# Kernel tuning notes

Measured on AMD Instinct MI355X. Metric: run time of the kernel, lower is better.

The kernel has to match this reference:

```python
import jax, jax.numpy as jnp
import numpy as np
from jax import lax

HEIGHT, WIDTH = 13, 10
HIDDEN = 256
CONV_OUT = 32 * 3 * 2  # 192, matches torch _get_conv_output_size


def setup_inputs() -> dict:
    key = jax.random.key(0)
    ks = jax.random.split(key, 12)
    B, T = 128, 512
    s = 0.05
    return {
        "x": jax.random.normal(ks[0], (B, T, HEIGHT, WIDTH), jnp.float32),
        "conv1_w": jax.random.normal(ks[1], (16, 1, 3, 3), jnp.float32) * s,
        "conv1_b": jax.random.normal(ks[2], (16,), jnp.float32) * s,
        "conv2_w": jax.random.normal(ks[3], (32, 16, 3, 3), jnp.float32) * s,
        "conv2_b": jax.random.normal(ks[4], (32,), jnp.float32) * s,
        "W_ih": jax.random.normal(ks[5], (4 * HIDDEN, CONV_OUT), jnp.float32) * s,
        "b_ih": jax.random.normal(ks[6], (4 * HIDDEN,), jnp.float32) * s,
        "W_hh": jax.random.normal(ks[7], (4 * HIDDEN, HIDDEN), jnp.float32) * s,
        "b_hh": jax.random.normal(ks[8], (4 * HIDDEN,), jnp.float32) * s,
        "cls_w": jax.random.normal(ks[9], (64, HIDDEN), jnp.float32) * s,
        "cls_b": jax.random.normal(ks[10], (64,), jnp.float32) * s,
    }


def _conv2d(x, w, b):
    # NCHW, OIHW, padding=1 (SAME for 3x3)
    y = lax.conv_general_dilated(x, w, window_strides=(1, 1),
                                 padding=((1, 1), (1, 1)),
                                 dimension_numbers=("NCHW", "OIHW", "NCHW"))
    return y + b[None, :, None, None]


def _maxpool2(x):
    # kernel 2, stride 2, VALID (floor) like nn.MaxPool2d(2)
    return lax.reduce_window(x, -jnp.inf, lax.max,
                             (1, 1, 2, 2), (1, 1, 2, 2), "VALID")


def reference(x, conv1_w, conv1_b, conv2_w, conv2_b, W_ih, b_ih, W_hh, b_hh, cls_w, cls_b):
    B, T, Hd, Wd = x.shape
    xi = x.reshape(B * T, 1, Hd, Wd)
    y = _maxpool2(jax.nn.relu(_conv2d(xi, conv1_w, conv1_b)))
    y = _maxpool2(jax.nn.relu(_conv2d(y, conv2_w, conv2_b)))
    feat = y.reshape(B, T, -1)  # [B, T, 192], channel-major flatten matches torch view

    # Precompute input contribution to gates for all steps (same math, batched)
    gx_all = jnp.einsum("btf,gf->btg", feat, W_ih) + b_ih + b_hh  # [B, T, 4H]
    H = W_hh.shape[1]

    def step(carry, gx):
        h, c = carry
        gates = gx + h @ W_hh.T  # [B, 4H]
        i, f, g, o = jnp.split(gates, 4, axis=1)
        i = jax.nn.sigmoid(i)
        f = jax.nn.sigmoid(f)
        g = jnp.tanh(g)
        o = jax.nn.sigmoid(o)
        c = f * c + i * g
        h = o * jnp.tanh(c)
        return (h, c), None

    h0 = jnp.zeros((B, H), x.dtype)
    c0 = jnp.zeros((B, H), x.dtype)
    (hT, _), _ = lax.scan(step, (h0, c0), jnp.swapaxes(gx_all, 0, 1))
    logits = hT @ cls_w.T + cls_b
    return logits
```

## Files before the change

kernel.cpp:

```cpp
#include <hip/hip_runtime.h>
#include <hip/hip_bf16.h>


typedef _Float16 half2v __attribute__((ext_vector_type(2)));
typedef _Float16 f16x8 __attribute__((ext_vector_type(8)));
typedef float f32x4 __attribute__((ext_vector_type(4)));

__device__ __forceinline__ float dot2f16(half2v a, half2v b, float c) {
#if defined(__has_builtin)
#if __has_builtin(__builtin_amdgcn_fdot2)
    return __builtin_amdgcn_fdot2(a, b, c, false);
#else
    return c + (float)a.x * (float)b.x + (float)a.y * (float)b.y;
#endif
#else
    return c + (float)a.x * (float)b.x + (float)a.y * (float)b.y;
#endif
}

__device__ __forceinline__ unsigned int packf2(const float* p) {
    half2v hv;
    hv.x = (_Float16)p[0];
    hv.y = (_Float16)p[1];
    return __builtin_bit_cast(unsigned int, hv);
}

__device__ __forceinline__ half2v bch2(unsigned int u) {
    return __builtin_bit_cast(half2v, u);
}

__global__ __launch_bounds__(256) void conv_kernel(
    const float* __restrict__ x,
    const float* __restrict__ c1w,
    const float* __restrict__ c1b,
    const float* __restrict__ c2w,
    const float* __restrict__ c2b,
    _Float16* __restrict__ feat)
{
    __shared__ float w1t[9 * 16];
    __shared__ float b1s[16];
    __shared__ float w2t[16 * 9 * 32];
    __shared__ float b2s[32];
    __shared__ float xp[4][14 * 12];
    __shared__ float p1p[4][16 * 8 * 7];

    const int tid = threadIdx.x;

    for (int idx = tid; idx < 144; idx += 256) {
        int oc = idx / 9, k = idx % 9;
        w1t[k * 16 + oc] = c1w[idx];
    }
    if (tid < 16) b1s[tid] = c1b[tid];
    for (int idx = tid; idx < 4608; idx += 256) {
        int oc = idx / 144, ic = (idx / 9) % 16, k = idx % 9;
        w2t[(ic * 9 + k) * 32 + oc] = c2w[idx];
    }
    if (tid < 32) b2s[tid] = c2b[tid];

    const int w = tid >> 6;
    const int lane = tid & 63;
    const int img = blockIdx.x * 4 + w;

    for (int i = lane; i < 14 * 12; i += 64) xp[w][i] = 0.f;
    for (int i = lane; i < 16 * 8 * 7; i += 64) p1p[w][i] = 0.f;
    __syncthreads();

    const float* xin = x + (size_t)img * 130;
    for (int i = lane; i < 130; i += 64) {
        int r = i / 10, c = i % 10;
        xp[w][(r + 1) * 12 + (c + 1)] = xin[i];
    }
    __syncthreads();

    {
        const int oc = lane & 15, q = lane >> 4;
        #pragma unroll
        for (int i = 0; i < 8; i++) {
            int pos = i * 4 + q;
            if (pos < 30) {
                int ph = pos / 5, pw = pos % 5;
                float cmax = -1e30f;
                #pragma unroll
                for (int pt = 0; pt < 4; pt++) {
                    int Y = 2 * ph + (pt >> 1), X = 2 * pw + (pt & 1);
                    float s = 0.f;
                    #pragma unroll
                    for (int k = 0; k < 9; k++) {
                        int dy = k / 3, dx = k % 3;
                        s += w1t[k * 16 + oc] * xp[w][(Y + dy) * 12 + X + dx];
                    }
                    cmax = fmaxf(cmax, s);
                }
                p1p[w][(oc * 8 + ph + 1) * 7 + (pw + 1)] = fmaxf(0.f, cmax + b1s[oc]);
            }
        }
    }
    __syncthreads();

    {
        const int oc = lane & 31, pw2 = lane >> 5;
        float acc[3][4];
        #pragma unroll
        for (int a = 0; a < 3; a++)
            #pragma unroll
            for (int b = 0; b < 4; b++) acc[a][b] = 0.f;

        for (int ic = 0; ic < 16; ic++) {
            #pragma unroll
            for (int k = 0; k < 9; k++) {
                int dy = k / 3, dx = k % 3;
                float wv = w2t[(ic * 9 + k) * 32 + oc];
                #pragma unroll
                for (int ph2 = 0; ph2 < 3; ph2++) {
                    #pragma unroll
                    for (int pt = 0; pt < 4; pt++) {
                        int y = 2 * ph2 + (pt >> 1) + dy;
                        int xx = 2 * pw2 + (pt & 1) + dx;
                        acc[ph2][pt] += wv * p1p[w][(ic * 8 + y) * 7 + xx];
                    }
                }
            }
        }
        float bias = b2s[oc];
        _Float16* fo = feat + (size_t)img * 192;
        #pragma unroll
        for (int ph2 = 0; ph2 < 3; ph2++) {
            float m = fmaxf(fmaxf(acc[ph2][0], acc[ph2][1]),
                            fmaxf(acc[ph2][2], acc[ph2][3]));
            fo[oc * 6 + ph2 * 2 + pw2] = (_Float16)fmaxf(0.f, m + bias);
        }
    }
}

__global__ __launch_bounds__(256) void gemm_gx_kernel(
    const _Float16* __restrict__ feat,
    const float* __restrict__ Wih,
    const float* __restrict__ bih,
    const float* __restrict__ bhh,
    _Float16* __restrict__ gx)
{
    __shared__ uint4 As4[64][25];
    __shared__ uint4 Bs4[64][25];

    const int tid = threadIdx.x;
    const int n0 = blockIdx.x * 64;
    const int m0 = blockIdx.y * 64;

    #pragma unroll
    for (int it = 0; it < 6; it++) {
        int q = tid + it * 256;
        int m = q / 24, c = q % 24;
        As4[m][c] = *(const uint4*)(feat + (size_t)(m0 + m) * 192 + c * 8);
    }
    unsigned int* Bu = (unsigned int*)Bs4;
    #pragma unroll
    for (int it = 0; it < 24; it++) {
        int q = tid + it * 256;
        int n = q / 96, p = q % 96;
        Bu[n * 100 + p] = packf2(Wih + (size_t)(n0 + n) * 192 + 2 * p);
    }
    __syncthreads();

    const int wv = tid >> 6;
    const int lane = tid & 63;
    const int lm = lane & 15;
    const int lk = lane >> 4;

    f32x4 acc[4] = {{0.f, 0.f, 0.f, 0.f}, {0.f, 0.f, 0.f, 0.f},
                    {0.f, 0.f, 0.f, 0.f}, {0.f, 0.f, 0.f, 0.f}};

    #pragma unroll
    for (int ks = 0; ks < 6; ks++) {
        f16x8 a = __builtin_bit_cast(f16x8, As4[wv * 16 + lm][ks * 4 + lk]);
        #pragma unroll
        for (int j = 0; j < 4; j++) {
            f16x8 b = __builtin_bit_cast(f16x8, Bs4[j * 16 + lm][ks * 4 + lk]);
            acc[j] = __builtin_amdgcn_mfma_f32_16x16x32_f16(a, b, acc[j], 0, 0, 0);
        }
    }

    #pragma unroll
    for (int j = 0; j < 4; j++) {
        int n = n0 + j * 16 + lm;
        float bias = bih[n] + bhh[n];
        #pragma unroll
        for (int i = 0; i < 4; i++) {
            int m = m0 + wv * 16 + lk * 4 + i;
            gx[(size_t)m * 1024 + n] = (_Float16)(acc[j][i] + bias);
        }
    }
}

__global__ __attribute__((amdgpu_flat_work_group_size(512, 512), amdgpu_waves_per_eu(2, 2)))
void lstm_kernel(
    const _Float16* __restrict__ gx,
    const float* __restrict__ Whh,
    const float* __restrict__ clsw,
    const float* __restrict__ clsb,
    float* __restrict__ out)
{
    __shared__ uint4 wl4[9][1024];
    __shared__ __align__(16) _Float16 hbuf[2][256];
    __shared__ float hfin[256];
    __shared__ float xg[512];

    const int t = threadIdx.x;
    const int b = blockIdx.x;
    const int r0 = t, r1 = t + 512;

    const float* w0 = Whh + (size_t)r0 * 256;
    const float* w1 = Whh + (size_t)r1 * 256;

    half2v wr0[92], wr1[92];
    #pragma unroll
    for (int p = 0; p < 92; p++) {
        wr0[p] = bch2(packf2(&w0[2 * p]));
        wr1[p] = bch2(packf2(&w1[2 * p]));
    }
    #pragma unroll
    for (int ch = 0; ch < 9; ch++) {
        uint4 v0, v1;
        v0.x = packf2(&w0[184 + 8 * ch + 0]);
        v0.y = packf2(&w0[184 + 8 * ch + 2]);
        v0.z = packf2(&w0[184 + 8 * ch + 4]);
        v0.w = packf2(&w0[184 + 8 * ch + 6]);
        v1.x = packf2(&w1[184 + 8 * ch + 0]);
        v1.y = packf2(&w1[184 + 8 * ch + 2]);
        v1.z = packf2(&w1[184 + 8 * ch + 4]);
        v1.w = packf2(&w1[184 + 8 * ch + 6]);
        wl4[ch][r0] = v0;
        wl4[ch][r1] = v1;
    }
    if (t < 256) hbuf[0][t] = (_Float16)0.f;
    __syncthreads();

    float c = 0.f;
    int cur = 0;
    const _Float16* gxb = gx + (size_t)b * 512 * 1024;
    float ga = (float)gxb[r0];
    float gb = (float)gxb[r1];

    for (int step = 0; step < 512; step++) {
        const _Float16* gxn = gxb + (size_t)((step + 1) & 511) * 1024;
        _Float16 na = gxn[r0];
        _Float16 nb = gxn[r1];

        float acc0 = ga, acc1 = gb;
        const unsigned int* hp = (const unsigned int*)&hbuf[cur][0];

        #pragma unroll
        for (int ch = 0; ch < 23; ch++) {
            uint4 hv = *(const uint4*)(hp + ch * 4);
            unsigned int hw[4] = {hv.x, hv.y, hv.z, hv.w};
            #pragma unroll
            for (int j = 0; j < 4; j++) {
                half2v h2 = bch2(hw[j]);
                acc0 = dot2f16(wr0[ch * 4 + j], h2, acc0);
                acc1 = dot2f16(wr1[ch * 4 + j], h2, acc1);
            }
        }
        #pragma unroll
        for (int ch = 0; ch < 9; ch++) {
            uint4 hv = *(const uint4*)(hp + 92 + 4 * ch);
            uint4 u0 = wl4[ch][r0];
            uint4 u1 = wl4[ch][r1];
            acc0 = dot2f16(bch2(u0.x), bch2(hv.x), acc0);
            acc0 = dot2f16(bch2(u0.y), bch2(hv.y), acc0);
            acc0 = dot2f16(bch2(u0.z), bch2(hv.z), acc0);
            acc0 = dot2f16(bch2(u0.w), bch2(hv.w), acc0);
            acc1 = dot2f16(bch2(u1.x), bch2(hv.x), acc1);
            acc1 = dot2f16(bch2(u1.y), bch2(hv.y), acc1);
            acc1 = dot2f16(bch2(u1.z), bch2(hv.z), acc1);
            acc1 = dot2f16(bch2(u1.w), bch2(hv.w), acc1);
        }

        if (t >= 256) {
            xg[t - 256] = acc0;
            xg[t] = acc1;
        }
        __syncthreads();
        if (t < 256) {
            float i_ = 1.f / (1.f + __expf(-acc0));
            float g_ = 1.f - 2.f / (__expf(2.f * acc1) + 1.f);
            float f_ = 1.f / (1.f + __expf(-xg[t]));
            float o_ = 1.f / (1.f + __expf(-xg[t + 256]));
            c = f_ * c + i_ * g_;
            float th = 1.f - 2.f / (__expf(2.f * c) + 1.f);
            float h = o_ * th;
            hbuf[cur ^ 1][t] = (_Float16)h;
            if (step == 511) hfin[t] = h;
        }
        __syncthreads();
        cur ^= 1;
        ga = (float)na;
        gb = (float)nb;
    }

    if (t < 64) {
        const float* wrow = clsw + t * 256;
        float s = clsb[t];
        for (int k = 0; k < 256; k++) s += wrow[k] * hfin[k];
        out[b * 64 + t] = s;
    }
}

extern "C" void kernel_launch(void* const* d_in, const int* in_sizes, int n_in,
                              void* d_out, int out_size, void* d_ws, size_t ws_size,
                              hipStream_t stream) {
    const float* x    = (const float*)d_in[0];
    const float* c1w  = (const float*)d_in[1];
    const float* c1b  = (const float*)d_in[2];
    const float* c2w  = (const float*)d_in[3];
    const float* c2b  = (const float*)d_in[4];
    const float* Wih  = (const float*)d_in[5];
    const float* bih  = (const float*)d_in[6];
    const float* Whh  = (const float*)d_in[7];
    const float* bhh  = (const float*)d_in[8];
    const float* clsw = (const float*)d_in[9];
    const float* clsb = (const float*)d_in[10];

    _Float16* feat = (_Float16*)d_ws;
    _Float16* gx   = feat + (size_t)65536 * 192;
    float* outp = (float*)d_out;

    hipLaunchKernelGGL(conv_kernel, dim3(16384), dim3(256), 0, stream,
                       x, c1w, c1b, c2w, c2b, feat);
    hipLaunchKernelGGL(gemm_gx_kernel, dim3(16, 1024), dim3(256), 0, stream,
                       feat, Wih, bih, bhh, gx);
    hipLaunchKernelGGL(lstm_kernel, dim3(128), dim3(512), 0, stream,
                       gx, Whh, clsw, clsb, outp);
}
```

Before: 1.329 ms.

## Use one thread per gate row and broadcast hidden state via readlane

The LSTM recurrence kernel now launches 1024 threads per block, one per W_hh row, instead of 512 threads each handling two rows. Every wave loads the hidden state once as a uint2 per lane and broadcasts it with readlane, replacing repeated LDS vector reads of h. Each thread keeps two accumulators that are summed into shared memory. The final h is read from the fp16 buffer instead of a separate fp32 copy, which slightly lowers classifier precision. Register pressure per thread is lower, but more waves contend for the per-step barriers, and readlane produces scalar values that can serialize issue.

```diff
diff --git a/kernel.cpp b/kernel.cpp
--- a/kernel.cpp
+++ b/kernel.cpp
@@ -191,8 +191,7 @@
     }
 }
 
-__global__ __attribute__((amdgpu_flat_work_group_size(512, 512), amdgpu_waves_per_eu(2, 2)))
-void lstm_kernel(
+__global__ __launch_bounds__(1024, 4) void lstm_kernel(
     const _Float16* __restrict__ gx,
     const float* __restrict__ Whh,
     const float* __restrict__ clsw,
@@ -201,35 +200,25 @@
 {
     __shared__ uint4 wl4[9][1024];
     __shared__ __align__(16) _Float16 hbuf[2][256];
-    __shared__ float hfin[256];
-    __shared__ float xg[512];
+    __shared__ float xg[1024];
 
     const int t = threadIdx.x;
     const int b = blockIdx.x;
-    const int r0 = t, r1 = t + 512;
-
-    const float* w0 = Whh + (size_t)r0 * 256;
-    const float* w1 = Whh + (size_t)r1 * 256;
-
-    half2v wr0[92], wr1[92];
-    #pragma unroll
-    for (int p = 0; p < 92; p++) {
-        wr0[p] = bch2(packf2(&w0[2 * p]));
-        wr1[p] = bch2(packf2(&w1[2 * p]));
-    }
+    const int lane = t & 63;
+
+    const float* wrow = Whh + (size_t)t * 256;
+
+    half2v wr[92];
+    #pragma unroll
+    for (int p = 0; p < 92; p++) wr[p] = bch2(packf2(&wrow[2 * p]));
     #pragma unroll
     for (int ch = 0; ch < 9; ch++) {
-        uint4 v0, v1;
-        v0.x = packf2(&w0[184 + 8 * ch + 0]);
-        v0.y = packf2(&w0[184 + 8 * ch + 2]);
-        v0.z = packf2(&w0[184 + 8 * ch + 4]);
-        v0.w = packf2(&w0[184 + 8 * ch + 6]);
-        v1.x = packf2(&w1[184 + 8 * ch + 0]);
-        v1.y = packf2(&w1[184 + 8 * ch + 2]);
-        v1.z = packf2(&w1[184 + 8 * ch + 4]);
-        v1.w = packf2(&w1[184 + 8 * ch + 6]);
-        wl4[ch][r0] = v0;
-        wl4[ch][r1] = v1;
+        uint4 v;
+        v.x = packf2(&wrow[184 + 8 * ch + 0]);
+        v.y = packf2(&wrow[184 + 8 * ch + 2]);
+        v.z = packf2(&wrow[184 + 8 * ch + 4]);
+        v.w = packf2(&wrow[184 + 8 * ch + 6]);
+        wl4[ch][t] = v;
     }
     if (t < 256) hbuf[0][t] = (_Float16)0.f;
     __syncthreads();
@@ -237,69 +226,57 @@
     float c = 0.f;
     int cur = 0;
     const _Float16* gxb = gx + (size_t)b * 512 * 1024;
-    float ga = (float)gxb[r0];
-    float gb = (float)gxb[r1];
+    float ga = (float)gxb[t];
 
     for (int step = 0; step < 512; step++) {
         const _Float16* gxn = gxb + (size_t)((step + 1) & 511) * 1024;
-        _Float16 na = gxn[r0];
-        _Float16 nb = gxn[r1];
-
-        float acc0 = ga, acc1 = gb;
-        const unsigned int* hp = (const unsigned int*)&hbuf[cur][0];
-
-        #pragma unroll
-        for (int ch = 0; ch < 23; ch++) {
-            uint4 hv = *(const uint4*)(hp + ch * 4);
-            unsigned int hw[4] = {hv.x, hv.y, hv.z, hv.w};
-            #pragma unroll
-            for (int j = 0; j < 4; j++) {
-                half2v h2 = bch2(hw[j]);
-                acc0 = dot2f16(wr0[ch * 4 + j], h2, acc0);
-                acc1 = dot2f16(wr1[ch * 4 + j], h2, acc1);
-            }
+        _Float16 na = gxn[t];
+
+        uint2 vh = *(const uint2*)&hbuf[cur][lane * 4];
+
+        float acc0 = ga, acc1 = 0.f;
+        #pragma unroll
+        for (int p = 0; p < 92; p += 2) {
+            unsigned int h0 = __builtin_amdgcn_readlane(vh.x, p >> 1);
+            unsigned int h1 = __builtin_amdgcn_readlane(vh.y, p >> 1);
+            acc0 = dot2f16(wr[p], bch2(h0), acc0);
+            acc1 = dot2f16(wr[p + 1], bch2(h1), acc1);
         }
         #pragma unroll
         for (int ch = 0; ch < 9; ch++) {
-            uint4 hv = *(const uint4*)(hp + 92 + 4 * ch);
-            uint4 u0 = wl4[ch][r0];
-            uint4 u1 = wl4[ch][r1];
-            acc0 = dot2f16(bch2(u0.x), bch2(hv.x), acc0);
-            acc0 = dot2f16(bch2(u0.y), bch2(hv.y), acc0);
-            acc0 = dot2f16(bch2(u0.z), bch2(hv.z), acc0);
-            acc0 = dot2f16(bch2(u0.w), bch2(hv.w), acc0);
-            acc1 = dot2f16(bch2(u1.x), bch2(hv.x), acc1);
-            acc1 = dot2f16(bch2(u1.y), bch2(hv.y), acc1);
-            acc1 = dot2f16(bch2(u1.z), bch2(hv.z), acc1);
-            acc1 = dot2f16(bch2(u1.w), bch2(hv.w), acc1);
-        }
-
-        if (t >= 256) {
-            xg[t - 256] = acc0;
-            xg[t] = acc1;
-        }
+            uint4 u = wl4[ch][t];
+            int p = 92 + 4 * ch;
+            unsigned int h0 = __builtin_amdgcn_readlane(vh.x, (p >> 1) + 0);
+            unsigned int h1 = __builtin_amdgcn_readlane(vh.y, (p >> 1) + 0);
+            unsigned int h2 = __builtin_amdgcn_readlane(vh.x, (p >> 1) + 1);
+            unsigned int h3 = __builtin_amdgcn_readlane(vh.y, (p >> 1) + 1);
+            acc0 = dot2f16(bch2(u.x), bch2(h0), acc0);
+            acc1 = dot2f16(bch2(u.y), bch2(h1), acc1);
+            acc0 = dot2f16(bch2(u.z), bch2(h2), acc0);
+            acc1 = dot2f16(bch2(u.w), bch2(h3), acc1);
+        }
+        xg[t] = acc0 + acc1;
         __syncthreads();
+
         if (t < 256) {
-            float i_ = 1.f / (1.f + __expf(-acc0));
-            float g_ = 1.f - 2.f / (__expf(2.f * acc1) + 1.f);
-            float f_ = 1.f / (1.f + __expf(-xg[t]));
-            float o_ = 1.f / (1.f + __expf(-xg[t + 256]));
+            float i_ = 1.f / (1.f + __expf(-xg[t]));
+            float f_ = 1.f / (1.f + __expf(-xg[t + 256]));
+            float g_ = 1.f - 2.f / (__expf(2.f * xg[t + 512]) + 1.f);
+            float o_ = 1.f / (1.f + __expf(-xg[t + 768]));
             c = f_ * c + i_ * g_;
             float th = 1.f - 2.f / (__expf(2.f * c) + 1.f);
             float h = o_ * th;
             hbuf[cur ^ 1][t] = (_Float16)h;
-            if (step == 511) hfin[t] = h;
         }
         __syncthreads();
         cur ^= 1;
         ga = (float)na;
-        gb = (float)nb;
     }
 
     if (t < 64) {
-        const float* wrow = clsw + t * 256;
+        const float* cw = clsw + t * 256;
         float s = clsb[t];
-        for (int k = 0; k < 256; k++) s += wrow[k] * hfin[k];
+        for (int k = 0; k < 256; k++) s += cw[k] * (float)hbuf[cur][k];
         out[b * 64 + t] = s;
     }
 }
@@ -327,6 +304,6 @@
                        x, c1w, c1b, c2w, c2b, feat);
     hipLaunchKernelGGL(gemm_gx_kernel, dim3(16, 1024), dim3(256), 0, stream,
                        feat, Wih, bih, bhh, gx);
-    hipLaunchKernelGGL(lstm_kernel, dim3(128), dim3(512), 0, stream,
+    hipLaunchKernelGGL(lstm_kernel, dim3(128), dim3(1024), 0, stream,
                        gx, Whh, clsw, clsb, outp);
 }
```

After: 1.677 ms. 26.2% more time.

## Split W_hh across registers, LDS and a prepacked fp16 global buffer in LSTM

Applied to the files above, without the earlier changes.

Adds a prepack kernel that converts part of W_hh (columns 152-255) to packed fp16 in workspace. The LSTM step now reads those columns from global/L2 every step, takes columns 0-71 from LDS and keeps only columns 72-151 in registers. This cuts per-thread register use from 184 to 80 halves, presumably to avoid spills, at the cost of extra global-memory traffic on the serial recurrence critical path. It also drops the fp32 hfin buffer and runs the classifier on the fp16 hidden state.

```diff
diff --git a/kernel.cpp b/kernel.cpp
--- a/kernel.cpp
+++ b/kernel.cpp
@@ -27,6 +27,25 @@
 
 __device__ __forceinline__ half2v bch2(unsigned int u) {
     return __builtin_bit_cast(half2v, u);
+}
+
+__device__ __forceinline__ uint4 pack8(const float* p) {
+    uint4 v;
+    v.x = packf2(p + 0);
+    v.y = packf2(p + 2);
+    v.z = packf2(p + 4);
+    v.w = packf2(p + 6);
+    return v;
+}
+
+__global__ __launch_bounds__(256) void prepack_kernel(
+    const float* __restrict__ Whh, uint4* __restrict__ sw)
+{
+    int idx = blockIdx.x * 256 + threadIdx.x;
+    if (idx < 13 * 1024) {
+        int c = idx >> 10, r = idx & 1023;
+        sw[idx] = pack8(Whh + (size_t)r * 256 + 152 + 8 * c);
+    }
 }
 
 __global__ __launch_bounds__(256) void conv_kernel(
@@ -191,17 +210,16 @@
     }
 }
 
-__global__ __attribute__((amdgpu_flat_work_group_size(512, 512), amdgpu_waves_per_eu(2, 2)))
-void lstm_kernel(
+__global__ __launch_bounds__(512, 2) void lstm_kernel(
     const _Float16* __restrict__ gx,
     const float* __restrict__ Whh,
+    const uint4* __restrict__ sw,
     const float* __restrict__ clsw,
     const float* __restrict__ clsb,
     float* __restrict__ out)
 {
     __shared__ uint4 wl4[9][1024];
     __shared__ __align__(16) _Float16 hbuf[2][256];
-    __shared__ float hfin[256];
     __shared__ float xg[512];
 
     const int t = threadIdx.x;
@@ -211,25 +229,16 @@
     const float* w0 = Whh + (size_t)r0 * 256;
     const float* w1 = Whh + (size_t)r1 * 256;
 
-    half2v wr0[92], wr1[92];
-    #pragma unroll
-    for (int p = 0; p < 92; p++) {
-        wr0[p] = bch2(packf2(&w0[2 * p]));
-        wr1[p] = bch2(packf2(&w1[2 * p]));
-    }
     #pragma unroll
     for (int ch = 0; ch < 9; ch++) {
-        uint4 v0, v1;
-        v0.x = packf2(&w0[184 + 8 * ch + 0]);
-        v0.y = packf2(&w0[184 + 8 * ch + 2]);
-        v0.z = packf2(&w0[184 + 8 * ch + 4]);
-        v0.w = packf2(&w0[184 + 8 * ch + 6]);
-        v1.x = packf2(&w1[184 + 8 * ch + 0]);
-        v1.y = packf2(&w1[184 + 8 * ch + 2]);
-        v1.z = packf2(&w1[184 + 8 * ch + 4]);
-        v1.w = packf2(&w1[184 + 8 * ch + 6]);
-        wl4[ch][r0] = v0;
-        wl4[ch][r1] = v1;
+        wl4[ch][r0] = pack8(w0 + 8 * ch);
+        wl4[ch][r1] = pack8(w1 + 8 * ch);
+    }
+    half2v wr0[40], wr1[40];
+    #pragma unroll
+    for (int q = 0; q < 40; q++) {
+        wr0[q] = bch2(packf2(w0 + 72 + 2 * q));
+        wr1[q] = bch2(packf2(w1 + 72 + 2 * q));
     }
     if (t < 256) hbuf[0][t] = (_Float16)0.f;
     __syncthreads();
@@ -246,24 +255,13 @@
         _Float16 nb = gxn[r1];
 
         float acc0 = ga, acc1 = gb;
-        const unsigned int* hp = (const unsigned int*)&hbuf[cur][0];
-
-        #pragma unroll
-        for (int ch = 0; ch < 23; ch++) {
-            uint4 hv = *(const uint4*)(hp + ch * 4);
-            unsigned int hw[4] = {hv.x, hv.y, hv.z, hv.w};
-            #pragma unroll
-            for (int j = 0; j < 4; j++) {
-                half2v h2 = bch2(hw[j]);
-                acc0 = dot2f16(wr0[ch * 4 + j], h2, acc0);
-                acc1 = dot2f16(wr1[ch * 4 + j], h2, acc1);
-            }
-        }
-        #pragma unroll
-        for (int ch = 0; ch < 9; ch++) {
-            uint4 hv = *(const uint4*)(hp + 92 + 4 * ch);
-            uint4 u0 = wl4[ch][r0];
-            uint4 u1 = wl4[ch][r1];
+        const uint4* hb4 = (const uint4*)&hbuf[cur][0];
+
+        #pragma unroll
+        for (int sc = 0; sc < 13; sc++) {
+            uint4 u0 = sw[sc * 1024 + r0];
+            uint4 u1 = sw[sc * 1024 + r1];
+            uint4 hv = hb4[19 + sc];
             acc0 = dot2f16(bch2(u0.x), bch2(hv.x), acc0);
             acc0 = dot2f16(bch2(u0.y), bch2(hv.y), acc0);
             acc0 = dot2f16(bch2(u0.z), bch2(hv.z), acc0);
@@ -272,6 +270,32 @@
             acc1 = dot2f16(bch2(u1.y), bch2(hv.y), acc1);
             acc1 = dot2f16(bch2(u1.z), bch2(hv.z), acc1);
             acc1 = dot2f16(bch2(u1.w), bch2(hv.w), acc1);
+        }
+        #pragma unroll
+        for (int ch = 0; ch < 9; ch++) {
+            uint4 u0 = wl4[ch][r0];
+            uint4 u1 = wl4[ch][r1];
+            uint4 hv = hb4[ch];
+            acc0 = dot2f16(bch2(u0.x), bch2(hv.x), acc0);
+            acc0 = dot2f16(bch2(u0.y), bch2(hv.y), acc0);
+            acc0 = dot2f16(bch2(u0.z), bch2(hv.z), acc0);
+            acc0 = dot2f16(bch2(u0.w), bch2(hv.w), acc0);
+            acc1 = dot2f16(bch2(u1.x), bch2(hv.x), acc1);
+            acc1 = dot2f16(bch2(u1.y), bch2(hv.y), acc1);
+            acc1 = dot2f16(bch2(u1.z), bch2(hv.z), acc1);
+            acc1 = dot2f16(bch2(u1.w), bch2(hv.w), acc1);
+        }
+        #pragma unroll
+        for (int cc = 0; cc < 10; cc++) {
+            uint4 hv = hb4[9 + cc];
+            acc0 = dot2f16(wr0[4 * cc + 0], bch2(hv.x), acc0);
+            acc0 = dot2f16(wr0[4 * cc + 1], bch2(hv.y), acc0);
+            acc0 = dot2f16(wr0[4 * cc + 2], bch2(hv.z), acc0);
+            acc0 = dot2f16(wr0[4 * cc + 3], bch2(hv.w), acc0);
+            acc1 = dot2f16(wr1[4 * cc + 0], bch2(hv.x), acc1);
+            acc1 = dot2f16(wr1[4 * cc + 1], bch2(hv.y), acc1);
+            acc1 = dot2f16(wr1[4 * cc + 2], bch2(hv.z), acc1);
+            acc1 = dot2f16(wr1[4 * cc + 3], bch2(hv.w), acc1);
         }
 
         if (t >= 256) {
@@ -288,7 +312,6 @@
             float th = 1.f - 2.f / (__expf(2.f * c) + 1.f);
             float h = o_ * th;
             hbuf[cur ^ 1][t] = (_Float16)h;
-            if (step == 511) hfin[t] = h;
         }
         __syncthreads();
         cur ^= 1;
@@ -297,9 +320,9 @@
     }
 
     if (t < 64) {
-        const float* wrow = clsw + t * 256;
+        const float* cw = clsw + t * 256;
         float s = clsb[t];
-        for (int k = 0; k < 256; k++) s += wrow[k] * hfin[k];
+        for (int k = 0; k < 256; k++) s += cw[k] * (float)hbuf[cur][k];
         out[b * 64 + t] = s;
     }
 }
@@ -321,12 +344,14 @@
 
     _Float16* feat = (_Float16*)d_ws;
     _Float16* gx   = feat + (size_t)65536 * 192;
+    uint4* sw      = (uint4*)(gx + (size_t)65536 * 1024);
     float* outp = (float*)d_out;
 
+    hipLaunchKernelGGL(prepack_kernel, dim3(52), dim3(256), 0, stream, Whh, sw);
     hipLaunchKernelGGL(conv_kernel, dim3(16384), dim3(256), 0, stream,
                        x, c1w, c1b, c2w, c2b, feat);
     hipLaunchKernelGGL(gemm_gx_kernel, dim3(16, 1024), dim3(256), 0, stream,
                        feat, Wih, bih, bhh, gx);
     hipLaunchKernelGGL(lstm_kernel, dim3(128), dim3(512), 0, stream,
-                       gx, Whh, clsw, clsb, outp);
-}
+                       gx, Whh, sw, clsw, clsb, outp);
+}
```

Result: faster. 1.293 ms (-2.7%).
